# Kernel tuning notes

Hardware: AMD Instinct MI355X
Metric: run time of the kernel (lower is better)

## Reference

```python
import jax, jax.numpy as jnp
import numpy as np

N_NODES = 16384
N_EDGES = 262144
N_GRAPHS = 64
COLORS = 16
EMB = 256
HEADS = 8
FFN = 1024
LAYERS = 4
LMAX = 320


def _ln(x, g, b, eps=1e-5):
    m = x.mean(-1, keepdims=True)
    v = x.var(-1, keepdims=True)
    return (x - m) * jax.lax.rsqrt(v + eps) * g + b


def setup_inputs() -> dict:
    key = jax.random.key(0)
    ks = iter(jax.random.split(key, 64))
    s = 0.05
    def rn(shape):
        return jax.random.normal(next(ks), shape, jnp.float32) * s
    # 64 graphs: 32 with 192 nodes, 32 with 320 nodes -> total 16384, L_max=320
    lengths = np.concatenate([np.full(32, 192, np.int64), np.full(32, 320, np.int64)])
    batches = jnp.asarray(np.concatenate([[0], np.cumsum(lengths)]).astype(np.int32))
    x = jax.random.normal(next(ks), (N_NODES, COLORS), jnp.float32)
    edge_index = jax.random.randint(next(ks), (2, N_EDGES), 0, N_NODES, jnp.int32)
    inp = dict(
        x=x, edge_index=edge_index, batches=batches, L_max=LMAX,
        sW0=rn((COLORS, EMB)), sWn0=rn((COLORS, EMB)), sb0=jnp.zeros(EMB),
        sW1=rn((EMB, EMB)), sWn1=rn((EMB, EMB)), sb1=jnp.zeros(EMB),
        sW2=rn((EMB, EMB)), sWn2=rn((EMB, EMB)), sb2=jnp.zeros(EMB),
        Wq=rn((LAYERS, EMB, EMB)), Wk=rn((LAYERS, EMB, EMB)), Wv=rn((LAYERS, EMB, EMB)),
        bq=jnp.zeros((LAYERS, EMB)), bk=jnp.zeros((LAYERS, EMB)), bv=jnp.zeros((LAYERS, EMB)),
        Wo=rn((LAYERS, EMB, EMB)), bo=jnp.zeros((LAYERS, EMB)),
        ln1g=jnp.ones((LAYERS, EMB)), ln1b=jnp.zeros((LAYERS, EMB)),
        ln2g=jnp.ones((LAYERS, EMB)), ln2b=jnp.zeros((LAYERS, EMB)),
        W1=rn((LAYERS, EMB, FFN)), b1=jnp.zeros((LAYERS, FFN)),
        W2=rn((LAYERS, FFN, EMB)), b2=jnp.zeros((LAYERS, EMB)),
    )
    return inp


def reference(x, edge_index, batches, L_max,
              sW0, sWn0, sb0, sW1, sWn1, sb1, sW2, sWn2, sb2,
              Wq, Wk, Wv, bq, bk, bv, Wo, bo,
              ln1g, ln1b, ln2g, ln2b, W1, b1, W2, b2):
    N = x.shape[0]
    src, dst = edge_index[0], edge_index[1]
    deg = jnp.maximum(
        jax.ops.segment_sum(jnp.ones(src.shape[0], x.dtype), dst, num_segments=N), 1.0
    )[:, None]

    def sage(h, Ws, Wn, b, act):
        agg = jax.ops.segment_sum(h[src], dst, num_segments=N) / deg  # mean neighbor agg
        h2 = h @ Ws + agg @ Wn + b
        return jax.nn.relu(h2) if act else h2

    z = sage(x, sW0, sWn0, sb0, True)
    z = sage(z, sW1, sWn1, sb1, True)
    z = sage(z, sW2, sWn2, sb2, False)

    # pack_and_pad (intended semantics): seq-first [L_max, n_graphs, D] + key padding mask
    nG = batches.shape[0] - 1
    lengths = batches[1:] - batches[:-1]
    ids = jnp.arange(N)
    seg = jnp.searchsorted(batches, ids, side='right') - 1  # graph id per node
    pos = ids - batches[seg]                                 # position within graph
    D = z.shape[1]
    h = jnp.zeros((L_max, nG, D), z.dtype).at[pos, seg].set(z)
    pad = jnp.arange(L_max)[None, :] >= lengths[:, None]     # [nG, L_max], True = padded

    H = HEADS
    dh = D // H
    scale = 1.0 / np.sqrt(dh).astype(np.float32)
    for l in range(Wq.shape[0]):
        L, Bg = h.shape[0], h.shape[1]
        q = (h @ Wq[l] + bq[l]).reshape(L, Bg, H, dh)
        k = (h @ Wk[l] + bk[l]).reshape(L, Bg, H, dh)
        v = (h @ Wv[l] + bv[l]).reshape(L, Bg, H, dh)
        sc = jnp.einsum('lbhd,mbhd->bhlm', q, k) * scale
        sc = jnp.where(pad[:, None, None, :], -1e9, sc)
        a = jax.nn.softmax(sc, axis=-1)
        o = jnp.einsum('bhlm,mbhd->lbhd', a, v).reshape(L, Bg, D) @ Wo[l] + bo[l]
        h = _ln(h + o, ln1g[l], ln1b[l])
        ff = jax.nn.relu(h @ W1[l] + b1[l]) @ W2[l] + b2[l]
        h = _ln(h + ff, ln2g[l], ln2b[l])
    return h
```

## Files before the change

kernel.cpp:

```cpp
#include <hip/hip_runtime.h>
#include <hip/hip_bf16.h>
#include <math.h>

#define NN  16384
#define NE  262144
#define NG  64
#define CIN 16
#define DD  256
#define NHD 8
#define DHD 32
#define DFF 1024
#define NLY 4
#define LM  320
#define NR  (LM*NG)
#define QS  768
#define QKW 512

typedef __attribute__((ext_vector_type(8))) short bf16x8;
typedef __attribute__((ext_vector_type(4))) float f32x4;

__device__ __forceinline__ unsigned short f2bf(float f) {
    union { __hip_bfloat16 h; unsigned short u; } cv;
    cv.h = __float2bfloat16(f);
    return cv.u;
}
__device__ __forceinline__ float bf2f(unsigned short u) {
    return __uint_as_float((unsigned int)u << 16);
}
__device__ __forceinline__ void gl_lds16(const unsigned short* g, unsigned short* l) {
    __builtin_amdgcn_global_load_lds(
        (const __attribute__((address_space(1))) unsigned int*)g,
        (__attribute__((address_space(3))) unsigned int*)l, 16, 0, 0);
}

__global__ void zero_ws_kernel(uint4* __restrict__ hb, int n16, int* __restrict__ counts) {
    int i = blockIdx.x * 256 + threadIdx.x;
    if (i < n16) hb[i] = (uint4){0u, 0u, 0u, 0u};
    if (i < NN) counts[i] = 0;
}

__global__ __launch_bounds__(256) void prep_all_kernel(
    const float* __restrict__ Wq, const float* __restrict__ Wk, const float* __restrict__ Wv,
    const float* __restrict__ Wo, const float* __restrict__ W1, const float* __restrict__ W2,
    const float* __restrict__ sW1, const float* __restrict__ sWn1,
    const float* __restrict__ sW2, const float* __restrict__ sWn2,
    const float* __restrict__ bq, const float* __restrict__ bk, const float* __restrict__ bv,
    unsigned short* __restrict__ Wqkvt, unsigned short* __restrict__ Wot,
    unsigned short* __restrict__ W1t, unsigned short* __restrict__ W2t,
    unsigned short* __restrict__ sW1t, unsigned short* __restrict__ sWn1t,
    unsigned short* __restrict__ sW2t, unsigned short* __restrict__ sWn2t,
    float* __restrict__ bqkvp)
{
    const int t = threadIdx.x;
    int bid = blockIdx.x;
    if (bid < 12) {
        int i = bid * 256 + t;
        if (i < NLY * QS) {
            int n = i % QS, l = i / QS;
            const float* b = (n < 256) ? bq : (n < 512 ? bk : bv);
            float v = b[l * DD + (n & 255)];
            if (n < 256) v *= 0.17677669529663687f;
            bqkvp[i] = v;
        }
        return;
    }
    bid -= 12;
    __shared__ float Ls[64][68];
    const float* inP;
    unsigned short* outP;
    int strideIn, strideOut;
    float sc = 1.f;
    if (bid < 192) {
        int x = bid % 12, y = (bid / 12) % 4, l = bid / 48;
        int n0 = x * 64, k0 = y * 64;
        const float* W = (n0 < 256) ? Wq : (n0 < 512 ? Wk : Wv);
        if (n0 < 256) sc = 0.17677669529663687f;
        inP  = W + ((size_t)l * DD + k0) * DD + (n0 & 255);
        strideIn = DD;
        outP = Wqkvt + ((size_t)l * QS + n0) * DD + k0;
        strideOut = DD;
    } else if (bid < 192 + 64) {
        bid -= 192;
        int x = bid % 4, y = (bid / 4) % 4, l = bid / 16;
        int n0 = x * 64, k0 = y * 64;
        inP  = Wo + ((size_t)l * DD + k0) * DD + n0;
        strideIn = DD;
        outP = Wot + ((size_t)l * DD + n0) * DD + k0;
        strideOut = DD;
    } else if (bid < 192 + 64 + 256) {
        bid -= 192 + 64;
        int x = bid % 16, y = (bid / 16) % 4, l = bid / 64;
        int n0 = x * 64, k0 = y * 64;
        inP  = W1 + ((size_t)l * DD + k0) * DFF + n0;
        strideIn = DFF;
        outP = W1t + ((size_t)l * DFF + n0) * DD + k0;
        strideOut = DD;
    } else if (bid < 192 + 64 + 512) {
        bid -= 192 + 64 + 256;
        int x = bid % 4, y = (bid / 4) % 16, l = bid / 64;
        int n0 = x * 64, k0 = y * 64;
        inP  = W2 + ((size_t)l * DFF + k0) * DD + n0;
        strideIn = DD;
        outP = W2t + ((size_t)l * DD + n0) * DFF + k0;
        strideOut = DFF;
    } else {
        bid -= 192 + 64 + 512;
        int w = bid / 16, r = bid % 16;
        int x = r % 4, y = r / 4;
        int n0 = x * 64, k0 = y * 64;
        const float* src = (w == 0) ? sW1 : (w == 1) ? sWn1 : (w == 2) ? sW2 : sWn2;
        unsigned short* dst = (w == 0) ? sW1t : (w == 1) ? sWn1t : (w == 2) ? sW2t : sWn2t;
        inP  = src + (size_t)k0 * DD + n0;
        strideIn = DD;
        outP = dst + (size_t)n0 * DD + k0;
        strideOut = DD;
    }
    #pragma unroll
    for (int it = 0; it < 4; ++it) {
        int lin = it * 256 + t;
        int kr = lin >> 4, nc = (lin & 15) * 4;
        float4 v = *(const float4*)&inP[(size_t)kr * strideIn + nc];
        Ls[kr][nc]     = v.x * sc;
        Ls[kr][nc + 1] = v.y * sc;
        Ls[kr][nc + 2] = v.z * sc;
        Ls[kr][nc + 3] = v.w * sc;
    }
    __syncthreads();
    #pragma unroll
    for (int it = 0; it < 2; ++it) {
        int lin = it * 256 + t;
        int nr = lin >> 3, kc = (lin & 7) * 8;
        unsigned short pk[8];
        #pragma unroll
        for (int j = 0; j < 8; ++j) pk[j] = f2bf(Ls[kc + j][nr]);
        *(uint4*)&outP[(size_t)nr * strideOut + kc] = *(uint4*)pk;
    }
}

__global__ void count_edges_kernel(const int* __restrict__ dst, int* __restrict__ counts) {
    int e = blockIdx.x * 256 + threadIdx.x;
    if (e < NE) atomicAdd(&counts[dst[e]], 1);
}

__global__ __launch_bounds__(1024) void scan_kernel(const int* __restrict__ counts,
                                                    int* __restrict__ offsets,
                                                    int* __restrict__ cursor) {
    __shared__ int part[1024];
    int t = threadIdx.x;
    int base = t * 16;
    int s = 0;
    #pragma unroll
    for (int i = 0; i < 16; ++i) s += counts[base + i];
    part[t] = s;
    __syncthreads();
    for (int off = 1; off < 1024; off <<= 1) {
        int val = (t >= off) ? part[t - off] : 0;
        __syncthreads();
        part[t] += val;
        __syncthreads();
    }
    int run = (t == 0) ? 0 : part[t - 1];
    #pragma unroll
    for (int i = 0; i < 16; ++i) {
        offsets[base + i] = run;
        cursor[base + i]  = run;
        run += counts[base + i];
    }
    if (t == 1023) offsets[NN] = run;
}

__global__ void fill_csr_kernel(const int* __restrict__ src, const int* __restrict__ dst,
                                int* __restrict__ cursor, int* __restrict__ csr) {
    int e = blockIdx.x * 256 + threadIdx.x;
    if (e < NE) {
        int p = atomicAdd(&cursor[dst[e]], 1);
        csr[p] = src[e];
    }
}

__global__ __launch_bounds__(256) void agg_mean16_kernel(
    const float* __restrict__ h, const int* __restrict__ offsets,
    const int* __restrict__ csr, float* __restrict__ out)
{
    int node = blockIdx.x * 16 + (threadIdx.x >> 4);
    int d = threadIdx.x & 15;
    int beg = offsets[node], end = offsets[node + 1];
    float acc = 0.f;
    for (int e = beg; e < end; ++e) acc += h[(size_t)csr[e] * CIN + d];
    int dg = end - beg; if (dg < 1) dg = 1;
    out[(size_t)node * CIN + d] = acc * (1.f / (float)dg);
}

__global__ __launch_bounds__(256) void agg_mean_b_kernel(
    const unsigned short* __restrict__ h, const int* __restrict__ offsets,
    const int* __restrict__ csr, unsigned short* __restrict__ out)
{
    int node = blockIdx.x * 4 + (threadIdx.x >> 6);
    int lane = threadIdx.x & 63;
    int beg = offsets[node], end = offsets[node + 1];
    float a0 = 0.f, a1 = 0.f, a2 = 0.f, a3 = 0.f;
    for (int e = beg; e < end; ++e) {
        const ushort4 hv = *(const ushort4*)(h + (size_t)csr[e] * DD + lane * 4);
        a0 += bf2f(hv.x); a1 += bf2f(hv.y); a2 += bf2f(hv.z); a3 += bf2f(hv.w);
    }
    int dg = end - beg; if (dg < 1) dg = 1;
    float inv = 1.f / (float)dg;
    ushort4 ov;
    ov.x = f2bf(a0 * inv); ov.y = f2bf(a1 * inv);
    ov.z = f2bf(a2 * inv); ov.w = f2bf(a3 * inv);
    *(ushort4*)(out + (size_t)node * DD + lane * 4) = ov;
}

template <int ACT, bool DUAL>
__global__ __launch_bounds__(256) void gemm_f32b_kernel(
    const float* __restrict__ A, const float* __restrict__ W,
    const float* __restrict__ A2, const float* __restrict__ W2,
    const float* __restrict__ bias, unsigned short* __restrict__ Cb,
    int M, int N, int K)
{
    __shared__ __align__(16) float As[16][64];
    __shared__ __align__(16) float Ws[16][64];
    const int t  = threadIdx.x;
    const int tx = t & 15, ty = t >> 4;
    const int m0 = blockIdx.y * 64, n0 = blockIdx.x * 64;
    const int arow = t >> 2, acol = (t & 3) * 4;
    const int wrow = t >> 4, wcol = (t & 15) * 4;
    float acc[4][4] = {};
    const int npass = DUAL ? 2 : 1;
    for (int pass = 0; pass < npass; ++pass) {
        const float* Ap = (DUAL && pass) ? A2 : A;
        const float* Wp = (DUAL && pass) ? W2 : W;
        for (int k0 = 0; k0 < K; k0 += 16) {
            __syncthreads();
            float4 av = *(const float4*)(Ap + (size_t)(m0 + arow) * K + k0 + acol);
            As[acol + 0][arow] = av.x;
            As[acol + 1][arow] = av.y;
            As[acol + 2][arow] = av.z;
            As[acol + 3][arow] = av.w;
            *(float4*)&Ws[wrow][wcol] = *(const float4*)(Wp + (size_t)(k0 + wrow) * N + n0 + wcol);
            __syncthreads();
            #pragma unroll
            for (int kk = 0; kk < 16; ++kk) {
                float4 a4 = *(const float4*)&As[kk][ty * 4];
                float4 b4 = *(const float4*)&Ws[kk][tx * 4];
                float aa[4] = {a4.x, a4.y, a4.z, a4.w};
                float bb[4] = {b4.x, b4.y, b4.z, b4.w};
                #pragma unroll
                for (int i = 0; i < 4; ++i)
                    #pragma unroll
                    for (int j = 0; j < 4; ++j)
                        acc[i][j] += aa[i] * bb[j];
            }
        }
    }
    float4 bv = *(const float4*)(bias + n0 + tx * 4);
    float bb4[4] = {bv.x, bv.y, bv.z, bv.w};
    #pragma unroll
    for (int i = 0; i < 4; ++i) {
        float c[4];
        #pragma unroll
        for (int j = 0; j < 4; ++j) {
            c[j] = acc[i][j] + bb4[j];
            if (ACT == 1) c[j] = fmaxf(c[j], 0.f);
        }
        ushort4 ov;
        ov.x = f2bf(c[0]); ov.y = f2bf(c[1]); ov.z = f2bf(c[2]); ov.w = f2bf(c[3]);
        *(ushort4*)(Cb + (size_t)(m0 + ty * 4 + i) * N + n0 + tx * 4) = ov;
    }
}

template <int ACT, bool DUAL, bool OUTF32, bool OUTBF16>
__global__ __launch_bounds__(256) void mfma_gemm_kernel(
    const unsigned short* __restrict__ A,  const unsigned short* __restrict__ Wt,
    const unsigned short* __restrict__ A2, const unsigned short* __restrict__ Wt2,
    const float* __restrict__ bias, float* __restrict__ Cf,
    unsigned short* __restrict__ Cb, int M, int N, int K)
{
    __shared__ __align__(16) unsigned short As[128 * 32];
    __shared__ __align__(16) unsigned short Bs[128 * 32];
    const int t = threadIdx.x;
    const int wave = t >> 6, lane = t & 63;
    const int quad = lane >> 4, r16 = lane & 15;
    const int wr = (wave >> 1) * 64, wc = (wave & 1) * 64;
    const int m0 = blockIdx.y * 128, n0 = blockIdx.x * 128;
    const int srow = t >> 2, sq = (t & 3) * 8;

    unsigned short* la = As + wave * 512;
    unsigned short* lb = Bs + wave * 512;

    f32x4 acc[4][4];
    #pragma unroll
    for (int i = 0; i < 4; ++i)
        #pragma unroll
        for (int j = 0; j < 4; ++j)
            acc[i][j] = (f32x4){0.f, 0.f, 0.f, 0.f};

    const int npass = DUAL ? 2 : 1;
    for (int pass = 0; pass < npass; ++pass) {
        const unsigned short* Ap = (DUAL && pass) ? A2 : A;
        const unsigned short* Wp = (DUAL && pass) ? Wt2 : Wt;
        for (int k0 = 0; k0 < K; k0 += 32) {
            __syncthreads();
            gl_lds16(&Ap[(size_t)(m0 + srow) * K + k0 + sq],       la);
            gl_lds16(&Ap[(size_t)(m0 + 64 + srow) * K + k0 + sq],  la + 2048);
            gl_lds16(&Wp[(size_t)(n0 + srow) * K + k0 + sq],       lb);
            gl_lds16(&Wp[(size_t)(n0 + 64 + srow) * K + k0 + sq],  lb + 2048);
            __syncthreads();
            bf16x8 af[4], bfr[4];
            #pragma unroll
            for (int i = 0; i < 4; ++i)
                af[i] = *(const bf16x8*)&As[(wr + i * 16 + r16) * 32 + quad * 8];
            #pragma unroll
            for (int j = 0; j < 4; ++j)
                bfr[j] = *(const bf16x8*)&Bs[(wc + j * 16 + r16) * 32 + quad * 8];
            #pragma unroll
            for (int i = 0; i < 4; ++i)
                #pragma unroll
                for (int j = 0; j < 4; ++j)
                    acc[i][j] = __builtin_amdgcn_mfma_f32_16x16x32_bf16(
                        af[i], bfr[j], acc[i][j], 0, 0, 0);
        }
    }

    float bcol[4];
    #pragma unroll
    for (int j = 0; j < 4; ++j) bcol[j] = bias[n0 + wc + j * 16 + r16];
    #pragma unroll
    for (int i = 0; i < 4; ++i) {
        const int rowb = m0 + wr + i * 16 + quad * 4;
        #pragma unroll
        for (int rr = 0; rr < 4; ++rr) {
            const size_t rb = (size_t)(rowb + rr) * N;
            #pragma unroll
            for (int j = 0; j < 4; ++j) {
                float v = acc[i][j][rr] + bcol[j];
                if (ACT == 1) v = fmaxf(v, 0.f);
                const int col = n0 + wc + j * 16 + r16;
                if (OUTF32) Cf[rb + col] = v;
                if (OUTBF16) Cb[rb + col] = f2bf(v);
            }
        }
    }
}

__global__ __launch_bounds__(256) void gemm_qkv_kernel(
    const unsigned short* __restrict__ A, const unsigned short* __restrict__ Wt,
    const float* __restrict__ bias, unsigned short* __restrict__ QKb,
    unsigned short* __restrict__ Vt, int K)
{
    __shared__ __align__(16) unsigned short As[128 * 32];
    __shared__ __align__(16) unsigned short Bs[128 * 32];
    const int t = threadIdx.x;
    const int wave = t >> 6, lane = t & 63;
    const int quad = lane >> 4, r16 = lane & 15;
    const int wr = (wave >> 1) * 64, wc = (wave & 1) * 64;
    const int m0 = blockIdx.y * 128, n0 = blockIdx.x * 128;
    const int srow = t >> 2, sq = (t & 3) * 8;
    unsigned short* la = As + wave * 512;
    unsigned short* lb = Bs + wave * 512;

    f32x4 acc[4][4];
    #pragma unroll
    for (int i = 0; i < 4; ++i)
        #pragma unroll
        for (int j = 0; j < 4; ++j)
            acc[i][j] = (f32x4){0.f, 0.f, 0.f, 0.f};

    for (int k0 = 0; k0 < K; k0 += 32) {
        __syncthreads();
        gl_lds16(&A[(size_t)(m0 + srow) * K + k0 + sq],       la);
        gl_lds16(&A[(size_t)(m0 + 64 + srow) * K + k0 + sq],  la + 2048);
        gl_lds16(&Wt[(size_t)(n0 + srow) * K + k0 + sq],      lb);
        gl_lds16(&Wt[(size_t)(n0 + 64 + srow) * K + k0 + sq], lb + 2048);
        __syncthreads();
        bf16x8 af[4], bfr[4];
        #pragma unroll
        for (int i = 0; i < 4; ++i)
            af[i] = *(const bf16x8*)&As[(wr + i * 16 + r16) * 32 + quad * 8];
        #pragma unroll
        for (int j = 0; j < 4; ++j)
            bfr[j] = *(const bf16x8*)&Bs[(wc + j * 16 + r16) * 32 + quad * 8];
        #pragma unroll
        for (int i = 0; i < 4; ++i)
            #pragma unroll
            for (int j = 0; j < 4; ++j)
                acc[i][j] = __builtin_amdgcn_mfma_f32_16x16x32_bf16(
                    af[i], bfr[j], acc[i][j], 0, 0, 0);
    }

    float bcol[4];
    #pragma unroll
    for (int j = 0; j < 4; ++j) bcol[j] = bias[n0 + wc + j * 16 + r16];

    if (n0 < 512) {
        #pragma unroll
        for (int i = 0; i < 4; ++i) {
            const int rowb = m0 + wr + i * 16 + quad * 4;
            #pragma unroll
            for (int rr = 0; rr < 4; ++rr) {
                const size_t rb = (size_t)(rowb + rr) * QKW;
                #pragma unroll
                for (int j = 0; j < 4; ++j)
                    QKb[rb + n0 + wc + j * 16 + r16] = f2bf(acc[i][j][rr] + bcol[j]);
            }
        }
    } else {
        #pragma unroll
        for (int i = 0; i < 4; ++i) {
            const int rowb = m0 + wr + i * 16 + quad * 4;
            const int g = rowb / LM;
            const int key = rowb - g * LM;
            #pragma unroll
            for (int j = 0; j < 4; ++j) {
                const int dim = n0 - 512 + wc + j * 16 + r16;
                unsigned short pk[4];
                #pragma unroll
                for (int rr = 0; rr < 4; ++rr) pk[rr] = f2bf(acc[i][j][rr] + bcol[j]);
                *(uint2*)&Vt[((size_t)g * DD + dim) * LM + key] = *(uint2*)pk;
            }
        }
    }
}

template <bool PERM>
__global__ __launch_bounds__(512) void gemm_ln_kernel(
    const unsigned short* __restrict__ A, const unsigned short* __restrict__ Wt,
    const float* __restrict__ bias, const unsigned short* __restrict__ residb,
    const float* __restrict__ gam, const float* __restrict__ bet,
    float* __restrict__ outF, unsigned short* __restrict__ outHb, int K)
{
    __shared__ __align__(16) unsigned short As[64 * 32];
    __shared__ __align__(16) unsigned short Bs[256 * 32];
    __shared__ float red[2][4][64];
    const int t = threadIdx.x;
    const int wave = t >> 6, lane = t & 63;
    const int quad = lane >> 4, r16 = lane & 15;
    const int wr = (wave >> 2) * 32;
    const int wc = (wave & 3) * 64;
    const int m0 = blockIdx.x * 64;
    const int srow = t >> 2, sq = (t & 3) * 8;

    f32x4 acc[2][4];
    #pragma unroll
    for (int i = 0; i < 2; ++i)
        #pragma unroll
        for (int j = 0; j < 4; ++j)
            acc[i][j] = (f32x4){0.f, 0.f, 0.f, 0.f};

    for (int k0 = 0; k0 < K; k0 += 32) {
        __syncthreads();
        if (wave < 4)
            gl_lds16(&A[(size_t)(m0 + srow) * K + k0 + sq], As + wave * 512);
        gl_lds16(&Wt[(size_t)srow * K + k0 + sq],         Bs + wave * 512);
        gl_lds16(&Wt[(size_t)(128 + srow) * K + k0 + sq], Bs + 4096 + wave * 512);
        __syncthreads();
        bf16x8 af[2], bfr[4];
        #pragma unroll
        for (int i = 0; i < 2; ++i)
            af[i] = *(const bf16x8*)&As[(wr + i * 16 + r16) * 32 + quad * 8];
        #pragma unroll
        for (int j = 0; j < 4; ++j)
            bfr[j] = *(const bf16x8*)&Bs[(wc + j * 16 + r16) * 32 + quad * 8];
        #pragma unroll
        for (int i = 0; i < 2; ++i)
            #pragma unroll
            for (int j = 0; j < 4; ++j)
                acc[i][j] = __builtin_amdgcn_mfma_f32_16x16x32_bf16(
                    af[i], bfr[j], acc[i][j], 0, 0, 0);
    }

    float bcol[4];
    #pragma unroll
    for (int j = 0; j < 4; ++j) bcol[j] = bias[wc + j * 16 + r16];

    #pragma unroll
    for (int i = 0; i < 2; ++i) {
        const int row = wr + i * 16 + quad * 4;
        #pragma unroll
        for (int rr = 0; rr < 4; ++rr) {
            const size_t rb = (size_t)(m0 + row + rr) * DD;
            float s1 = 0.f, s2 = 0.f;
            #pragma unroll
            for (int j = 0; j < 4; ++j) {
                float v = acc[i][j][rr] + bcol[j] + bf2f(residb[rb + wc + j * 16 + r16]);
                acc[i][j][rr] = v;
                s1 += v;
                s2 += v * v;
            }
            #pragma unroll
            for (int off = 1; off < 16; off <<= 1) {
                s1 += __shfl_xor(s1, off, 64);
                s2 += __shfl_xor(s2, off, 64);
            }
            if (r16 == 0) {
                red[0][wave & 3][row + rr] = s1;
                red[1][wave & 3][row + rr] = s2;
            }
        }
    }
    __syncthreads();
    #pragma unroll
    for (int i = 0; i < 2; ++i) {
        const int row = wr + i * 16 + quad * 4;
        #pragma unroll
        for (int rr = 0; rr < 4; ++rr) {
            const int lr = row + rr;
            const int gr = m0 + lr;
            float s1 = red[0][0][lr] + red[0][1][lr] + red[0][2][lr] + red[0][3][lr];
            float s2 = red[1][0][lr] + red[1][1][lr] + red[1][2][lr] + red[1][3][lr];
            float mean = s1 * (1.f / 256.f);
            float var  = s2 * (1.f / 256.f) - mean * mean;
            float rs = rsqrtf(var + 1e-5f);
            const size_t hb = (size_t)gr * DD;
            size_t fb = 0;
            if (PERM) {
                int gg = gr / LM, pos = gr - gg * LM;
                fb = ((size_t)pos * NG + gg) * DD;
            }
            #pragma unroll
            for (int j = 0; j < 4; ++j) {
                const int col = wc + j * 16 + r16;
                float ov = (acc[i][j][rr] - mean) * rs * gam[col] + bet[col];
                if (PERM) outF[fb + col] = ov;
                else      outHb[hb + col] = f2bf(ov);
            }
        }
    }
}

__global__ __launch_bounds__(256) void pack_kernel(
    const float* __restrict__ z, const int* __restrict__ batches,
    unsigned short* __restrict__ Hb)
{
    int node = blockIdx.x * 4 + (threadIdx.x >> 6);
    int lane = threadIdx.x & 63;
    int lo = 0, hi = NG;
    while (lo < hi) {
        int mid = (lo + hi + 1) >> 1;
        if (batches[mid] <= node) lo = mid; else hi = mid - 1;
    }
    int pos = node - batches[lo];
    size_t base = ((size_t)lo * LM + pos) * DD + lane * 4;
    float4 zv = *(const float4*)(z + (size_t)node * DD + lane * 4);
    ushort4 hb;
    hb.x = f2bf(zv.x); hb.y = f2bf(zv.y); hb.z = f2bf(zv.z); hb.w = f2bf(zv.w);
    *(ushort4*)(Hb + base) = hb;
}

__global__ __launch_bounds__(256) void attn_mfma_kernel(
    const unsigned short* __restrict__ qk, const unsigned short* __restrict__ vt,
    const int* __restrict__ batches, unsigned short* __restrict__ o)
{
    __shared__ __align__(16) unsigned short Pa[4][64 * 40];
    const int bx = blockIdx.x;
    const int g = bx & 63;
    const int r = bx >> 6;
    const int q0 = (r >> 1) * 64;
    const int tid = threadIdx.x;
    const int wave = tid >> 6;
    const int h = (r & 1) * 4 + wave;
    const int lane = tid & 63;
    const int quad = lane >> 4, r16 = lane & 15;
    const int len = batches[g + 1] - batches[g];
    const size_t gq = (size_t)g * LM;
    unsigned short* pa = Pa[wave];

    bf16x8 qf[4];
    #pragma unroll
    for (int i = 0; i < 4; ++i)
        qf[i] = *(const bf16x8*)(qk + (gq + q0 + i * 16 + r16) * QKW + h * 32 + quad * 8);
    bf16x8 onesf;
    #pragma unroll
    for (int j = 0; j < 8; ++j) onesf[j] = (short)0x3F80;

    f32x4 oacc[4][2], lacc[4];
    #pragma unroll
    for (int i = 0; i < 4; ++i) {
        lacc[i] = (f32x4){0.f, 0.f, 0.f, 0.f};
        #pragma unroll
        for (int nt = 0; nt < 2; ++nt)
            oacc[i][nt] = (f32x4){0.f, 0.f, 0.f, 0.f};
    }

    for (int t0 = 0; t0 < len; t0 += 32) {
        bf16x8 kf[2], vf[2];
        #pragma unroll
        for (int mt = 0; mt < 2; ++mt) {
            int kr = t0 + mt * 16 + r16; if (kr > LM - 1) kr = LM - 1;
            kf[mt] = *(const bf16x8*)(qk + (gq + kr) * QKW + 256 + h * 32 + quad * 8);
        }
        #pragma unroll
        for (int nt = 0; nt < 2; ++nt)
            vf[nt] = *(const bf16x8*)(vt + ((size_t)g * DD + h * 32 + nt * 16 + r16) * LM
                                      + t0 + quad * 8);
        f32x4 st[2][4];
        #pragma unroll
        for (int mt = 0; mt < 2; ++mt)
            #pragma unroll
            for (int i = 0; i < 4; ++i)
                st[mt][i] = (f32x4){0.f, 0.f, 0.f, 0.f};
        #pragma unroll
        for (int mt = 0; mt < 2; ++mt)
            #pragma unroll
            for (int i = 0; i < 4; ++i)
                st[mt][i] = __builtin_amdgcn_mfma_f32_16x16x32_bf16(
                    kf[mt], qf[i], st[mt][i], 0, 0, 0);
        #pragma unroll
        for (int i = 0; i < 4; ++i) {
            #pragma unroll
            for (int mt = 0; mt < 2; ++mt) {
                float pr[4];
                #pragma unroll
                for (int rr = 0; rr < 4; ++rr) {
                    int key = t0 + mt * 16 + quad * 4 + rr;
                    pr[rr] = (key < len) ? __expf(st[mt][i][rr]) : 0.f;
                }
                uint2 w;
                w.x = ((unsigned)f2bf(pr[1]) << 16) | f2bf(pr[0]);
                w.y = ((unsigned)f2bf(pr[3]) << 16) | f2bf(pr[2]);
                *(uint2*)&pa[(i * 16 + r16) * 40 + mt * 16 + quad * 4] = w;
            }
        }
        __asm__ volatile("s_waitcnt lgkmcnt(0)" ::: "memory");
        bf16x8 pf[4];
        #pragma unroll
        for (int i = 0; i < 4; ++i)
            pf[i] = *(const bf16x8*)&pa[(i * 16 + r16) * 40 + quad * 8];
        #pragma unroll
        for (int i = 0; i < 4; ++i) {
            #pragma unroll
            for (int nt = 0; nt < 2; ++nt)
                oacc[i][nt] = __builtin_amdgcn_mfma_f32_16x16x32_bf16(
                    pf[i], vf[nt], oacc[i][nt], 0, 0, 0);
            lacc[i] = __builtin_amdgcn_mfma_f32_16x16x32_bf16(
                pf[i], onesf, lacc[i], 0, 0, 0);
        }
    }
    #pragma unroll
    for (int i = 0; i < 4; ++i) {
        #pragma unroll
        for (int rr = 0; rr < 4; ++rr) {
            float inv = 1.f / lacc[i][rr];
            size_t base = (gq + q0 + i * 16 + quad * 4 + rr) * DD + h * 32;
            #pragma unroll
            for (int nt = 0; nt < 2; ++nt)
                o[base + nt * 16 + r16] = f2bf(oacc[i][nt][rr] * inv);
        }
    }
}

extern "C" void kernel_launch(void* const* d_in, const int* in_sizes, int n_in,
                              void* d_out, int out_size, void* d_ws, size_t ws_size,
                              hipStream_t stream) {
    const float* x       = (const float*)d_in[0];
    const int*   ei      = (const int*)d_in[1];
    const int*   batches = (const int*)d_in[2];
    const float* sW0  = (const float*)d_in[4];
    const float* sWn0 = (const float*)d_in[5];
    const float* sb0  = (const float*)d_in[6];
    const float* sW1  = (const float*)d_in[7];
    const float* sWn1 = (const float*)d_in[8];
    const float* sb1  = (const float*)d_in[9];
    const float* sW2  = (const float*)d_in[10];
    const float* sWn2 = (const float*)d_in[11];
    const float* sb2  = (const float*)d_in[12];
    const float* Wq   = (const float*)d_in[13];
    const float* Wk   = (const float*)d_in[14];
    const float* Wv   = (const float*)d_in[15];
    const float* bq   = (const float*)d_in[16];
    const float* bk   = (const float*)d_in[17];
    const float* bv   = (const float*)d_in[18];
    const float* Wo   = (const float*)d_in[19];
    const float* bo   = (const float*)d_in[20];
    const float* ln1g = (const float*)d_in[21];
    const float* ln1b = (const float*)d_in[22];
    const float* ln2g = (const float*)d_in[23];
    const float* ln2b = (const float*)d_in[24];
    const float* W1   = (const float*)d_in[25];
    const float* b1   = (const float*)d_in[26];
    const float* W2   = (const float*)d_in[27];
    const float* b2   = (const float*)d_in[28];

    char* p = (char*)d_ws;
    auto alloc = [&](size_t bytes) {
        char* r = p;
        p += (bytes + 255) & ~(size_t)255;
        return r;
    };
    int*   counts  = (int*)alloc((size_t)NN * 4);
    int*   offsets = (int*)alloc((size_t)(NN + 1) * 4);
    int*   cursor  = (int*)alloc((size_t)NN * 4);
    int*   csr     = (int*)alloc((size_t)NE * 4);
    float* agg0    = (float*)alloc((size_t)NN * CIN * 4);
    unsigned short* z0b = (unsigned short*)alloc((size_t)NN * DD * 2);
    unsigned short* a1b = (unsigned short*)alloc((size_t)NN * DD * 2);
    unsigned short* z1b = (unsigned short*)alloc((size_t)NN * DD * 2);
    unsigned short* a2b = (unsigned short*)alloc((size_t)NN * DD * 2);
    float* z2f     = (float*)alloc((size_t)NN * DD * 4);
    unsigned short* Vt = (unsigned short*)z2f;
    unsigned short* Hb = (unsigned short*)alloc((size_t)NR * DD * 2);
    unsigned short* Ob = (unsigned short*)alloc((size_t)NR * DD * 2);
    float* R       = (float*)alloc((size_t)NR * DFF * 2);
    unsigned short* QKb = (unsigned short*)R;
    unsigned short* F1b = (unsigned short*)R;
    unsigned short* Wqkvt = (unsigned short*)alloc((size_t)NLY * QS * DD * 2);
    unsigned short* Wot   = (unsigned short*)alloc((size_t)NLY * DD * DD * 2);
    unsigned short* W1t   = (unsigned short*)alloc((size_t)NLY * DFF * DD * 2);
    unsigned short* W2t   = (unsigned short*)alloc((size_t)NLY * DD * DFF * 2);
    unsigned short* sW1t  = (unsigned short*)alloc((size_t)DD * DD * 2);
    unsigned short* sWn1t = (unsigned short*)alloc((size_t)DD * DD * 2);
    unsigned short* sW2t  = (unsigned short*)alloc((size_t)DD * DD * 2);
    unsigned short* sWn2t = (unsigned short*)alloc((size_t)DD * DD * 2);
    float* bqkvp   = (float*)alloc((size_t)NLY * QS * 4);

    prep_all_kernel<<<844, 256, 0, stream>>>(
        Wq, Wk, Wv, Wo, W1, W2, sW1, sWn1, sW2, sWn2, bq, bk, bv,
        Wqkvt, Wot, W1t, W2t, sW1t, sWn1t, sW2t, sWn2t, bqkvp);
    zero_ws_kernel<<<(NR * DD / 8 + 255) / 256, 256, 0, stream>>>(
        (uint4*)Hb, NR * DD / 8, counts);

    count_edges_kernel<<<NE / 256, 256, 0, stream>>>(ei + NE, counts);
    scan_kernel<<<1, 1024, 0, stream>>>(counts, offsets, cursor);
    fill_csr_kernel<<<NE / 256, 256, 0, stream>>>(ei, ei + NE, cursor, csr);

    agg_mean16_kernel<<<NN / 16, 256, 0, stream>>>(x, offsets, csr, agg0);
    gemm_f32b_kernel<1, true><<<dim3(DD / 64, NN / 64), 256, 0, stream>>>(
        x, sW0, agg0, sWn0, sb0, z0b, NN, DD, CIN);
    agg_mean_b_kernel<<<NN / 4, 256, 0, stream>>>(z0b, offsets, csr, a1b);
    mfma_gemm_kernel<1, true, false, true><<<dim3(DD / 128, NN / 128), 256, 0, stream>>>(
        z0b, sW1t, a1b, sWn1t, sb1, nullptr, z1b, NN, DD, DD);
    agg_mean_b_kernel<<<NN / 4, 256, 0, stream>>>(z1b, offsets, csr, a2b);
    mfma_gemm_kernel<0, true, true, false><<<dim3(DD / 128, NN / 128), 256, 0, stream>>>(
        z1b, sW2t, a2b, sWn2t, sb2, z2f, nullptr, NN, DD, DD);

    pack_kernel<<<NN / 4, 256, 0, stream>>>(z2f, batches, Hb);

    for (int l = 0; l < NLY; ++l) {
        gemm_qkv_kernel<<<dim3(QS / 128, NR / 128), 256, 0, stream>>>(
            Hb, Wqkvt + (size_t)l * QS * DD, bqkvp + (size_t)l * QS, QKb, Vt, DD);
        attn_mfma_kernel<<<NG * 10, 256, 0, stream>>>(QKb, Vt, batches, Ob);
        gemm_ln_kernel<false><<<NR / 64, 512, 0, stream>>>(
            Ob, Wot + (size_t)l * DD * DD, bo + (size_t)l * DD, Hb,
            ln1g + (size_t)l * DD, ln1b + (size_t)l * DD, nullptr, Hb, DD);
        mfma_gemm_kernel<1, false, false, true><<<dim3(DFF / 128, NR / 128), 256, 0, stream>>>(
            Hb, W1t + (size_t)l * DFF * DD, nullptr, nullptr,
            b1 + (size_t)l * DFF, nullptr, F1b, NR, DFF, DD);
        if (l == NLY - 1)
            gemm_ln_kernel<true><<<NR / 64, 512, 0, stream>>>(
                F1b, W2t + (size_t)l * DD * DFF, b2 + (size_t)l * DD, Hb,
                ln2g + (size_t)l * DD, ln2b + (size_t)l * DD, (float*)d_out, Hb, DFF);
        else
            gemm_ln_kernel<false><<<NR / 64, 512, 0, stream>>>(
                F1b, W2t + (size_t)l * DD * DFF, b2 + (size_t)l * DD, Hb,
                ln2g + (size_t)l * DD, ln2b + (size_t)l * DD, nullptr, Hb, DFF);
    }
}
```

Measured before the change: 785.6 us.

## Double GEMM K-tile to 64 with XOR-swizzled LDS, widen neighbor aggregation loads

The three MFMA GEMM kernels (generic, QKV, GEMM+LayerNorm) now stage a K-slice of 64 per iteration instead of 32. The LDS tiles use an XOR swizzle on the column offset to avoid bank conflicts, which halves the number of barrier pairs per K. The bf16 neighbor-mean aggregation now has each half-wave take alternate edges with 16-byte loads and combines the halves with a shuffle. The small 16-wide aggregation is unrolled by two. LDS use doubles per block, which may reduce occupancy.

```diff
diff --git a/kernel.cpp b/kernel.cpp
--- a/kernel.cpp
+++ b/kernel.cpp
@@ -186,7 +186,13 @@
     int d = threadIdx.x & 15;
     int beg = offsets[node], end = offsets[node + 1];
     float acc = 0.f;
-    for (int e = beg; e < end; ++e) acc += h[(size_t)csr[e] * CIN + d];
+    int e = beg;
+    for (; e + 1 < end; e += 2) {
+        float v0 = h[(size_t)csr[e] * CIN + d];
+        float v1 = h[(size_t)csr[e + 1] * CIN + d];
+        acc += v0 + v1;
+    }
+    if (e < end) acc += h[(size_t)csr[e] * CIN + d];
     int dg = end - beg; if (dg < 1) dg = 1;
     out[(size_t)node * CIN + d] = acc * (1.f / (float)dg);
 }
@@ -197,18 +203,34 @@
 {
     int node = blockIdx.x * 4 + (threadIdx.x >> 6);
     int lane = threadIdx.x & 63;
+    int half = lane >> 5;
+    int hl   = lane & 31;
     int beg = offsets[node], end = offsets[node + 1];
-    float a0 = 0.f, a1 = 0.f, a2 = 0.f, a3 = 0.f;
-    for (int e = beg; e < end; ++e) {
-        const ushort4 hv = *(const ushort4*)(h + (size_t)csr[e] * DD + lane * 4);
-        a0 += bf2f(hv.x); a1 += bf2f(hv.y); a2 += bf2f(hv.z); a3 += bf2f(hv.w);
-    }
+    float a[8] = {0.f, 0.f, 0.f, 0.f, 0.f, 0.f, 0.f, 0.f};
+    int e = beg + half;
+    for (; e + 2 < end; e += 4) {
+        bf16x8 h0 = *(const bf16x8*)(h + (size_t)csr[e] * DD + hl * 8);
+        bf16x8 h1 = *(const bf16x8*)(h + (size_t)csr[e + 2] * DD + hl * 8);
+        #pragma unroll
+        for (int j = 0; j < 8; ++j) a[j] += bf2f((unsigned short)h0[j]);
+        #pragma unroll
+        for (int j = 0; j < 8; ++j) a[j] += bf2f((unsigned short)h1[j]);
+    }
+    if (e < end) {
+        bf16x8 h0 = *(const bf16x8*)(h + (size_t)csr[e] * DD + hl * 8);
+        #pragma unroll
+        for (int j = 0; j < 8; ++j) a[j] += bf2f((unsigned short)h0[j]);
+    }
+    #pragma unroll
+    for (int j = 0; j < 8; ++j) a[j] += __shfl_xor(a[j], 32, 64);
     int dg = end - beg; if (dg < 1) dg = 1;
     float inv = 1.f / (float)dg;
-    ushort4 ov;
-    ov.x = f2bf(a0 * inv); ov.y = f2bf(a1 * inv);
-    ov.z = f2bf(a2 * inv); ov.w = f2bf(a3 * inv);
-    *(ushort4*)(out + (size_t)node * DD + lane * 4) = ov;
+    if (half == 0) {
+        unsigned short pk[8];
+        #pragma unroll
+        for (int j = 0; j < 8; ++j) pk[j] = f2bf(a[j] * inv);
+        *(uint4*)(out + (size_t)node * DD + hl * 8) = *(uint4*)pk;
+    }
 }
 
 template <int ACT, bool DUAL>
@@ -276,17 +298,16 @@
     const float* __restrict__ bias, float* __restrict__ Cf,
     unsigned short* __restrict__ Cb, int M, int N, int K)
 {
-    __shared__ __align__(16) unsigned short As[128 * 32];
-    __shared__ __align__(16) unsigned short Bs[128 * 32];
+    __shared__ __align__(16) unsigned short As[128 * 64];
+    __shared__ __align__(16) unsigned short Bs[128 * 64];
     const int t = threadIdx.x;
     const int wave = t >> 6, lane = t & 63;
     const int quad = lane >> 4, r16 = lane & 15;
     const int wr = (wave >> 1) * 64, wc = (wave & 1) * 64;
     const int m0 = blockIdx.y * 128, n0 = blockIdx.x * 128;
-    const int srow = t >> 2, sq = (t & 3) * 8;
-
-    unsigned short* la = As + wave * 512;
-    unsigned short* lb = Bs + wave * 512;
+    const int srow = t >> 3;
+    const int scol = ((t & 7) * 8) ^ ((srow & 7) << 3);
+    const int swz  = (r16 & 7) << 3;
 
     f32x4 acc[4][4];
     #pragma unroll
@@ -299,26 +320,33 @@
     for (int pass = 0; pass < npass; ++pass) {
         const unsigned short* Ap = (DUAL && pass) ? A2 : A;
         const unsigned short* Wp = (DUAL && pass) ? Wt2 : Wt;
-        for (int k0 = 0; k0 < K; k0 += 32) {
+        for (int k0 = 0; k0 < K; k0 += 64) {
             __syncthreads();
-            gl_lds16(&Ap[(size_t)(m0 + srow) * K + k0 + sq],       la);
-            gl_lds16(&Ap[(size_t)(m0 + 64 + srow) * K + k0 + sq],  la + 2048);
-            gl_lds16(&Wp[(size_t)(n0 + srow) * K + k0 + sq],       lb);
-            gl_lds16(&Wp[(size_t)(n0 + 64 + srow) * K + k0 + sq],  lb + 2048);
+            #pragma unroll
+            for (int c = 0; c < 4; ++c) {
+                gl_lds16(&Ap[(size_t)(m0 + c * 32 + srow) * K + k0 + scol],
+                         As + c * 2048 + wave * 512);
+                gl_lds16(&Wp[(size_t)(n0 + c * 32 + srow) * K + k0 + scol],
+                         Bs + c * 2048 + wave * 512);
+            }
             __syncthreads();
-            bf16x8 af[4], bfr[4];
-            #pragma unroll
-            for (int i = 0; i < 4; ++i)
-                af[i] = *(const bf16x8*)&As[(wr + i * 16 + r16) * 32 + quad * 8];
-            #pragma unroll
-            for (int j = 0; j < 4; ++j)
-                bfr[j] = *(const bf16x8*)&Bs[(wc + j * 16 + r16) * 32 + quad * 8];
-            #pragma unroll
-            for (int i = 0; i < 4; ++i)
+            #pragma unroll
+            for (int kk = 0; kk < 2; ++kk) {
+                const int cofs = (kk * 32 + quad * 8) ^ swz;
+                bf16x8 af[4], bfr[4];
+                #pragma unroll
+                for (int i = 0; i < 4; ++i)
+                    af[i] = *(const bf16x8*)&As[(wr + i * 16 + r16) * 64 + cofs];
                 #pragma unroll
                 for (int j = 0; j < 4; ++j)
-                    acc[i][j] = __builtin_amdgcn_mfma_f32_16x16x32_bf16(
-                        af[i], bfr[j], acc[i][j], 0, 0, 0);
+                    bfr[j] = *(const bf16x8*)&Bs[(wc + j * 16 + r16) * 64 + cofs];
+                #pragma unroll
+                for (int i = 0; i < 4; ++i)
+                    #pragma unroll
+                    for (int j = 0; j < 4; ++j)
+                        acc[i][j] = __builtin_amdgcn_mfma_f32_16x16x32_bf16(
+                            af[i], bfr[j], acc[i][j], 0, 0, 0);
+            }
         }
     }
 
@@ -348,16 +376,16 @@
     const float* __restrict__ bias, unsigned short* __restrict__ QKb,
     unsigned short* __restrict__ Vt, int K)
 {
-    __shared__ __align__(16) unsigned short As[128 * 32];
-    __shared__ __align__(16) unsigned short Bs[128 * 32];
+    __shared__ __align__(16) unsigned short As[128 * 64];
+    __shared__ __align__(16) unsigned short Bs[128 * 64];
     const int t = threadIdx.x;
     const int wave = t >> 6, lane = t & 63;
     const int quad = lane >> 4, r16 = lane & 15;
     const int wr = (wave >> 1) * 64, wc = (wave & 1) * 64;
     const int m0 = blockIdx.y * 128, n0 = blockIdx.x * 128;
-    const int srow = t >> 2, sq = (t & 3) * 8;
-    unsigned short* la = As + wave * 512;
-    unsigned short* lb = Bs + wave * 512;
+    const int srow = t >> 3;
+    const int scol = ((t & 7) * 8) ^ ((srow & 7) << 3);
+    const int swz  = (r16 & 7) << 3;
 
     f32x4 acc[4][4];
     #pragma unroll
@@ -366,26 +394,33 @@
         for (int j = 0; j < 4; ++j)
             acc[i][j] = (f32x4){0.f, 0.f, 0.f, 0.f};
 
-    for (int k0 = 0; k0 < K; k0 += 32) {
+    for (int k0 = 0; k0 < K; k0 += 64) {
         __syncthreads();
-        gl_lds16(&A[(size_t)(m0 + srow) * K + k0 + sq],       la);
-        gl_lds16(&A[(size_t)(m0 + 64 + srow) * K + k0 + sq],  la + 2048);
-        gl_lds16(&Wt[(size_t)(n0 + srow) * K + k0 + sq],      lb);
-        gl_lds16(&Wt[(size_t)(n0 + 64 + srow) * K + k0 + sq], lb + 2048);
+        #pragma unroll
+        for (int c = 0; c < 4; ++c) {
+            gl_lds16(&A[(size_t)(m0 + c * 32 + srow) * K + k0 + scol],
+                     As + c * 2048 + wave * 512);
+            gl_lds16(&Wt[(size_t)(n0 + c * 32 + srow) * K + k0 + scol],
+                     Bs + c * 2048 + wave * 512);
+        }
         __syncthreads();
-        bf16x8 af[4], bfr[4];
-        #pragma unroll
-        for (int i = 0; i < 4; ++i)
-            af[i] = *(const bf16x8*)&As[(wr + i * 16 + r16) * 32 + quad * 8];
-        #pragma unroll
-        for (int j = 0; j < 4; ++j)
-            bfr[j] = *(const bf16x8*)&Bs[(wc + j * 16 + r16) * 32 + quad * 8];
-        #pragma unroll
-        for (int i = 0; i < 4; ++i)
+        #pragma unroll
+        for (int kk = 0; kk < 2; ++kk) {
+            const int cofs = (kk * 32 + quad * 8) ^ swz;
+            bf16x8 af[4], bfr[4];
+            #pragma unroll
+            for (int i = 0; i < 4; ++i)
+                af[i] = *(const bf16x8*)&As[(wr + i * 16 + r16) * 64 + cofs];
             #pragma unroll
             for (int j = 0; j < 4; ++j)
-                acc[i][j] = __builtin_amdgcn_mfma_f32_16x16x32_bf16(
-                    af[i], bfr[j], acc[i][j], 0, 0, 0);
+                bfr[j] = *(const bf16x8*)&Bs[(wc + j * 16 + r16) * 64 + cofs];
+            #pragma unroll
+            for (int i = 0; i < 4; ++i)
+                #pragma unroll
+                for (int j = 0; j < 4; ++j)
+                    acc[i][j] = __builtin_amdgcn_mfma_f32_16x16x32_bf16(
+                        af[i], bfr[j], acc[i][j], 0, 0, 0);
+        }
     }
 
     float bcol[4];
@@ -429,8 +464,8 @@
     const float* __restrict__ gam, const float* __restrict__ bet,
     float* __restrict__ outF, unsigned short* __restrict__ outHb, int K)
 {
-    __shared__ __align__(16) unsigned short As[64 * 32];
-    __shared__ __align__(16) unsigned short Bs[256 * 32];
+    __shared__ __align__(16) unsigned short As[64 * 64];
+    __shared__ __align__(16) unsigned short Bs[256 * 64];
     __shared__ float red[2][4][64];
     const int t = threadIdx.x;
     const int wave = t >> 6, lane = t & 63;
@@ -438,7 +473,9 @@
     const int wr = (wave >> 2) * 32;
     const int wc = (wave & 3) * 64;
     const int m0 = blockIdx.x * 64;
-    const int srow = t >> 2, sq = (t & 3) * 8;
+    const int srow = t >> 3;
+    const int scol = ((t & 7) * 8) ^ ((srow & 7) << 3);
+    const int swz  = (r16 & 7) << 3;
 
     f32x4 acc[2][4];
     #pragma unroll
@@ -447,26 +484,31 @@
         for (int j = 0; j < 4; ++j)
             acc[i][j] = (f32x4){0.f, 0.f, 0.f, 0.f};
 
-    for (int k0 = 0; k0 < K; k0 += 32) {
+    for (int k0 = 0; k0 < K; k0 += 64) {
         __syncthreads();
-        if (wave < 4)
-            gl_lds16(&A[(size_t)(m0 + srow) * K + k0 + sq], As + wave * 512);
-        gl_lds16(&Wt[(size_t)srow * K + k0 + sq],         Bs + wave * 512);
-        gl_lds16(&Wt[(size_t)(128 + srow) * K + k0 + sq], Bs + 4096 + wave * 512);
+        gl_lds16(&A[(size_t)(m0 + srow) * K + k0 + scol], As + wave * 512);
+        #pragma unroll
+        for (int c = 0; c < 4; ++c)
+            gl_lds16(&Wt[(size_t)(c * 64 + srow) * K + k0 + scol],
+                     Bs + c * 4096 + wave * 512);
         __syncthreads();
-        bf16x8 af[2], bfr[4];
-        #pragma unroll
-        for (int i = 0; i < 2; ++i)
-            af[i] = *(const bf16x8*)&As[(wr + i * 16 + r16) * 32 + quad * 8];
-        #pragma unroll
-        for (int j = 0; j < 4; ++j)
-            bfr[j] = *(const bf16x8*)&Bs[(wc + j * 16 + r16) * 32 + quad * 8];
-        #pragma unroll
-        for (int i = 0; i < 2; ++i)
+        #pragma unroll
+        for (int kk = 0; kk < 2; ++kk) {
+            const int cofs = (kk * 32 + quad * 8) ^ swz;
+            bf16x8 af[2], bfr[4];
+            #pragma unroll
+            for (int i = 0; i < 2; ++i)
+                af[i] = *(const bf16x8*)&As[(wr + i * 16 + r16) * 64 + cofs];
             #pragma unroll
             for (int j = 0; j < 4; ++j)
-                acc[i][j] = __builtin_amdgcn_mfma_f32_16x16x32_bf16(
-                    af[i], bfr[j], acc[i][j], 0, 0, 0);
+                bfr[j] = *(const bf16x8*)&Bs[(wc + j * 16 + r16) * 64 + cofs];
+            #pragma unroll
+            for (int i = 0; i < 2; ++i)
+                #pragma unroll
+                for (int j = 0; j < 4; ++j)
+                    acc[i][j] = __builtin_amdgcn_mfma_f32_16x16x32_bf16(
+                        af[i], bfr[j], acc[i][j], 0, 0, 0);
+        }
     }
 
     float bcol[4];
```

Measured after the change: 702.2 us. 1.12x faster.
